# Kernel tuning notes

Hardware: AMD Instinct MI355X
Metric: run time of the kernel (lower is better)

## Reference

```python
import jax, jax.numpy as jnp
import numpy as np

MODEL_DIM = 2048
NUM_HEADS = 16
HEAD_DIM = MODEL_DIM // NUM_HEADS  # 128
B, L = 2, 2048


def _rope_tables(seq_len, head_dim, theta=10000.0):
    inv = 1.0 / (theta ** (np.arange(0, head_dim, 2)[: head_dim // 2].astype(np.float32) / head_dim))
    t = np.arange(seq_len, dtype=np.float32)
    freqs = np.outer(t, inv)  # [L, head_dim//2]
    return jnp.asarray(np.cos(freqs)), jnp.asarray(np.sin(freqs))


def setup_inputs() -> dict:
    key = jax.random.key(0)
    k1, k2, k3 = jax.random.split(key, 3)
    x = jax.random.normal(k1, (B, L, MODEL_DIM), dtype=jnp.float32)
    Wqkv = jax.random.normal(k2, (MODEL_DIM, 3 * MODEL_DIM), dtype=jnp.float32) / np.sqrt(MODEL_DIM)
    Wc = jax.random.normal(k3, (MODEL_DIM, MODEL_DIM), dtype=jnp.float32) / np.sqrt(MODEL_DIM)
    bc = jnp.zeros((MODEL_DIM,), dtype=jnp.float32)
    freqs_cos, freqs_sin = _rope_tables(L, HEAD_DIM)
    return {"x": x, "freqs_cos": freqs_cos, "freqs_sin": freqs_sin,
            "Wqkv": Wqkv, "Wc": Wc, "bc": bc}


def _apply_rope(t, cos, sin):
    # t: [B, L, H, hd] viewed as pairs (even, odd) along last dim; complex multiply by cis
    b, l, h, d = t.shape
    tp = t.reshape(b, l, h, d // 2, 2)
    te, to = tp[..., 0], tp[..., 1]
    cos = cos[None, :, None, :]  # [1, L, 1, d/2]
    sin = sin[None, :, None, :]
    oe = te * cos - to * sin
    oo = te * sin + to * cos
    return jnp.stack([oe, oo], axis=-1).reshape(b, l, h, d)


def reference(x, freqs_cos, freqs_sin, Wqkv, Wc, bc):
    b, l, d = x.shape
    qkv = x @ Wqkv  # [B, L, 3D]
    q, k, v = jnp.split(qkv, 3, axis=-1)
    q = q.reshape(b, l, NUM_HEADS, HEAD_DIM)
    k = k.reshape(b, l, NUM_HEADS, HEAD_DIM)
    v = v.reshape(b, l, NUM_HEADS, HEAD_DIM)
    q = _apply_rope(q, freqs_cos, freqs_sin)
    k = _apply_rope(k, freqs_cos, freqs_sin)
    scale = 1.0 / np.sqrt(HEAD_DIM).astype(np.float32)
    # causal SDPA: [B, H, Lq, Lk]
    scores = jnp.einsum('bqhd,bkhd->bhqk', q, k) * scale
    causal = jnp.tril(jnp.ones((l, l), dtype=bool))
    scores = jnp.where(causal[None, None], scores, jnp.finfo(scores.dtype).min)
    attn = jax.nn.softmax(scores, axis=-1)
    out = jnp.einsum('bhqk,bkhd->bqhd', attn, v).reshape(b, l, d)
    return out @ Wc + bc
```

## Files before the change

### kernel.cpp

```cpp
#include <hip/hip_runtime.h>
#include <hip/hip_bf16.h>

#define MODEL 2048
#define NHEAD 16
#define HDIM  128
#define BB    2
#define LL    2048
#define N1    (3*MODEL)
#define MTOT  (BB*LL)

typedef __hip_bfloat16 bf16;
typedef __attribute__((ext_vector_type(8))) short bf16x8;
typedef __attribute__((ext_vector_type(4))) float f32x4;

static __device__ __forceinline__ f32x4 mfma16(bf16x8 a, bf16x8 b, f32x4 c) {
  return __builtin_amdgcn_mfma_f32_16x16x32_bf16(a, b, c, 0, 0, 0);
}

static __device__ __forceinline__ void gl_lds16(const void* g, void* l) {
  __builtin_amdgcn_global_load_lds(
      (const __attribute__((address_space(1))) unsigned int*)g,
      (__attribute__((address_space(3))) unsigned int*)l, 16, 0, 0);
}

static __device__ __forceinline__ unsigned bfu(float x) {
  bf16 b = __float2bfloat16(x);
  return (unsigned)*reinterpret_cast<unsigned short*>(&b);
}

__global__ void k_cvt(const float* __restrict__ in, bf16* __restrict__ out, int n4) {
  int i = blockIdx.x * blockDim.x + threadIdx.x;
  if (i < n4) {
    float4 v = ((const float4*)in)[i];
    bf16* o = out + (size_t)i * 4;
    o[0] = __float2bfloat16(v.x);
    o[1] = __float2bfloat16(v.y);
    o[2] = __float2bfloat16(v.z);
    o[3] = __float2bfloat16(v.w);
  }
}

__global__ __launch_bounds__(256)
void k_transpose(const float* __restrict__ in, bf16* __restrict__ out, int R, int C) {
  __shared__ float t[32][33];
  const int c0 = blockIdx.x * 32, r0 = blockIdx.y * 32;
  const int tx = threadIdx.x & 31;
  const int ty = threadIdx.x >> 5;
#pragma unroll
  for (int i = 0; i < 4; ++i)
    t[ty + 8*i][tx] = in[(size_t)(r0 + ty + 8*i) * C + c0 + tx];
  __syncthreads();
#pragma unroll
  for (int i = 0; i < 4; ++i)
    out[(size_t)(c0 + ty + 8*i) * R + r0 + tx] = __float2bfloat16(t[tx][ty + 8*i]);
}


#define BARRIER __builtin_amdgcn_s_barrier()
#define SCHED0  __builtin_amdgcn_sched_barrier(0)
#define PRIO1 __builtin_amdgcn_s_setprio(1)
#define PRIO0 __builtin_amdgcn_s_setprio(0)

template<int EPI>
__global__ __launch_bounds__(512, 4)
void k_gemmP(const bf16* __restrict__ A, const bf16* __restrict__ BT,
             int M, int N, int K,
             float* __restrict__ Cout, const float* __restrict__ bias,
             bf16* __restrict__ Qb, bf16* __restrict__ Kb, bf16* __restrict__ VTb,
             const float* __restrict__ cosT, const float* __restrict__ sinT)
{
  constexpr int ABUF = 8192;
  constexpr int BBUF = 8192;
  constexpr int AREG = 3 * ABUF;
  extern __shared__ char smem[];

  const int tid = threadIdx.x;
  const int wid = tid >> 6, lane = tid & 63;
  const int wm = wid >> 2, wn = wid & 3;
  const int lr = lane & 15, lkg = lane >> 4;

  const int nbx = N >> 7;
  const int xcd = blockIdx.x & 7;
  const int i   = blockIdx.x >> 3;
  const int m0 = (((xcd >> 1) << 3) + (i & 7)) << 7;
  const int n0 = ((xcd & 1) * (nbx >> 1) + (i >> 3)) << 7;

  const int scol = ((lane & 3) ^ ((lane >> 3) & 3)) * 8;
  const bf16* Asrc = A  + (size_t)(m0 + wid*16 + (lane >> 2)) * K + scol;
  const bf16* Bsrc = BT + (size_t)(n0 + wid*16 + (lane >> 2)) * K + scol;

  auto stageA = [&](int t) {
    gl_lds16(Asrc + t*32, smem + (t % 3)*ABUF + wid*1024);
  };
  auto stageB = [&](int t) {
    gl_lds16(Bsrc + t*32, smem + AREG + (t % 3)*BBUF + wid*1024);
  };

  const int slotX = (lkg ^ ((lr >> 1) & 3)) * 16;
  const int aBase = wm*4096 + lr*64 + slotX;
  const int bBase = wn*2048 + lr*64 + slotX;

  const f32x4 vzero = {0.f, 0.f, 0.f, 0.f};
  f32x4 acc[4][2];
#pragma unroll
  for (int ii = 0; ii < 4; ++ii)
#pragma unroll
    for (int j = 0; j < 2; ++j) acc[ii][j] = vzero;

  const int nt = K >> 5;

  stageA(0); stageB(0); stageA(1); stageB(1);
  asm volatile("s_waitcnt vmcnt(2)" ::: "memory");
  SCHED0; BARRIER;

  for (int t = 0; t < nt; ++t) {
    const int bufA = (t % 3) * ABUF;
    const int bufB = AREG + (t % 3) * BBUF;
    const int ts   = (t + 2 < nt) ? t + 2 : nt - 1;
    bf16x8 aFr[4], bFr[2];

#pragma unroll
    for (int mf = 0; mf < 4; ++mf)
      aFr[mf] = *(const bf16x8*)(smem + bufA + aBase + mf*1024);
#pragma unroll
    for (int nf = 0; nf < 2; ++nf)
      bFr[nf] = *(const bf16x8*)(smem + bufB + bBase + nf*1024);
    stageA(ts); stageB(ts);

    asm volatile("s_waitcnt lgkmcnt(0)" ::: "memory");
    SCHED0;
    PRIO1;
#pragma unroll
    for (int mf = 0; mf < 4; ++mf)
#pragma unroll
      for (int nf = 0; nf < 2; ++nf)
        acc[mf][nf] = mfma16(aFr[mf], bFr[nf], acc[mf][nf]);
    PRIO0;
    asm volatile("s_waitcnt vmcnt(2)" ::: "memory");
    SCHED0;
    BARRIER;
  }

  if constexpr (EPI == 1) {
    const float inv_sqrt_d = 0.08838834764831845f;
#pragma unroll
    for (int nf = 0; nf < 2; ++nf) {
      const int gcb = n0 + wn*32 + nf*16;
      const int section = gcb >> 11;
      const int cc = (gcb & 2047) + lr;
      const int h = cc >> 7, d = cc & 127;
#pragma unroll
      for (int mf = 0; mf < 4; ++mf) {
#pragma unroll
        for (int reg = 0; reg < 4; ++reg) {
          const int grow = m0 + wm*64 + mf*16 + lkg*4 + reg;
          const int bidx = grow >> 11, lseq = grow & 2047;
          float val = acc[mf][nf][reg];
          if (section < 2) {
            float p = __shfl_xor(val, 1);
            const int fi = d >> 1;
            float cv = cosT[(size_t)lseq * 64 + fi];
            float sv = sinT[(size_t)lseq * 64 + fi];
            float r = (d & 1) ? fmaf(p, sv, val * cv)
                              : fmaf(val, cv, -p * sv);
            if (section == 0) {
              r *= inv_sqrt_d;
              Qb[((size_t)(bidx*NHEAD + h) * LL + lseq) * HDIM + d] = __float2bfloat16(r);
            } else {
              Kb[((size_t)(bidx*NHEAD + h) * LL + lseq) * HDIM + d] = __float2bfloat16(r);
            }
          } else {
            VTb[((size_t)(bidx*NHEAD + h) * HDIM + d) * LL + lseq] = __float2bfloat16(val);
          }
        }
      }
    }
  } else {
#pragma unroll
    for (int nf = 0; nf < 2; ++nf) {
      const int gcol = n0 + wn*32 + nf*16 + lr;
      const float bv = bias[gcol];
#pragma unroll
      for (int mf = 0; mf < 4; ++mf) {
#pragma unroll
        for (int reg = 0; reg < 4; ++reg) {
          const int grow = m0 + wm*64 + mf*16 + lkg*4 + reg;
          Cout[(size_t)grow * N + gcol] = acc[mf][nf][reg] + bv;
        }
      }
    }
  }
}

__global__ __launch_bounds__(256, 2)
void k_attn(const bf16* __restrict__ Qb, const bf16* __restrict__ Kb,
            const bf16* __restrict__ VTb, bf16* __restrict__ attnA)
{
  __shared__ bf16 Ks[64][136];
  __shared__ bf16 Vs[128][72];
  __shared__ bf16 Ps[4][32][72];

  const int bh  = blockIdx.y;
  const int bx  = blockIdx.x;
  const int tid = threadIdx.x;
  const int wid = tid >> 6, lane = tid & 63;
  const int lr  = lane & 15, lkg = lane >> 4;

  const bf16* Qh = Qb  + (size_t)bh * LL * HDIM;
  const bf16* Kh = Kb  + (size_t)bh * LL * HDIM;
  const bf16* Vh = VTb + (size_t)bh * HDIM * LL;
  const int b = bh >> 4, h = bh & 15;
  const f32x4 vzero = {0.f, 0.f, 0.f, 0.f};

  for (int pp = 0; pp < 2; ++pp) {
    const int qt  = pp ? bx : (15 - bx);
    const int Q0  = qt * 128;
    const int q0w = Q0 + wid * 32;

    bf16x8 qf[2][4];
#pragma unroll
    for (int qr = 0; qr < 2; ++qr)
#pragma unroll
      for (int kk = 0; kk < 4; ++kk)
        qf[qr][kk] = *(const bf16x8*)(Qh + (size_t)(q0w + qr*16 + lr) * HDIM + kk*32 + lkg*8);

    f32x4 oacc[2][8];
#pragma unroll
    for (int qr = 0; qr < 2; ++qr)
#pragma unroll
      for (int db = 0; db < 8; ++db) oacc[qr][db] = vzero;
    float ml[2] = {-INFINITY, -INFINITY};
    float ll[2] = {0.f, 0.f};

    const int NT = Q0 / 64 + 2;
    bf16x8 kpre[4], vpre[4];
#pragma unroll
    for (int j = 0; j < 4; ++j) {
      const int c = j*256 + tid;
      kpre[j] = *(const bf16x8*)(Kh + (size_t)(c >> 4) * HDIM + (c & 15) * 8);
      vpre[j] = *(const bf16x8*)(Vh + (size_t)(c >> 3) * LL + (c & 7) * 8);
    }

    for (int kt = 0; kt < NT; ++kt) {
      const int kbase = kt * 64;
      __syncthreads();
#pragma unroll
      for (int j = 0; j < 4; ++j) {
        const int c = j*256 + tid;
        *(bf16x8*)&Ks[c >> 4][(c & 15) * 8] = kpre[j];
        *(bf16x8*)&Vs[c >> 3][(c & 7) * 8]  = vpre[j];
      }
      __syncthreads();
      if (kt + 1 < NT) {
#pragma unroll
        for (int j = 0; j < 4; ++j) {
          const int c = j*256 + tid;
          kpre[j] = *(const bf16x8*)(Kh + (size_t)((kt+1)*64 + (c >> 4)) * HDIM + (c & 15) * 8);
          vpre[j] = *(const bf16x8*)(Vh + (size_t)(c >> 3) * LL + (kt+1)*64 + (c & 7) * 8);
        }
      }
      if (kbase <= q0w + 31) {
        f32x4 s2[2][4];
#pragma unroll
        for (int qr = 0; qr < 2; ++qr)
#pragma unroll
          for (int c = 0; c < 4; ++c) s2[qr][c] = vzero;
#pragma unroll
        for (int c = 0; c < 4; ++c) {
          bf16x8 kf[4];
#pragma unroll
          for (int kk = 0; kk < 4; ++kk)
            kf[kk] = *(const bf16x8*)&Ks[c*16 + lr][kk*32 + lkg*8];
#pragma unroll
          for (int qr = 0; qr < 2; ++qr)
#pragma unroll
            for (int kk = 0; kk < 4; ++kk)
              s2[qr][c] = mfma16(kf[kk], qf[qr][kk], s2[qr][c]);
        }
#pragma unroll
        for (int qr = 0; qr < 2; ++qr) {
          const int qrow = q0w + qr*16 + lr;
          float pv[4][4];
#pragma unroll
          for (int c = 0; c < 4; ++c)
#pragma unroll
            for (int reg = 0; reg < 4; ++reg) {
              const int kv = kbase + c*16 + lkg*4 + reg;
              pv[c][reg] = (kv <= qrow) ? s2[qr][c][reg] : -INFINITY;
            }
          float tm = pv[0][0];
#pragma unroll
          for (int c = 0; c < 4; ++c)
#pragma unroll
            for (int reg = 0; reg < 4; ++reg)
              if (c || reg) tm = fmaxf(tm, pv[c][reg]);
          tm = fmaxf(tm, __shfl_xor(tm, 16));
          tm = fmaxf(tm, __shfl_xor(tm, 32));
          const float mnew = fmaxf(ml[qr], tm);
          const float scl  = __expf(ml[qr] - mnew);
          ml[qr] = mnew;
          float rs = 0.f;
#pragma unroll
          for (int c = 0; c < 4; ++c)
#pragma unroll
            for (int reg = 0; reg < 4; ++reg) {
              pv[c][reg] = __expf(pv[c][reg] - mnew);
              rs += pv[c][reg];
            }
          rs += __shfl_xor(rs, 16);
          rs += __shfl_xor(rs, 32);
          ll[qr] = ll[qr] * scl + rs;
#pragma unroll
          for (int c = 0; c < 4; ++c) {
            unsigned lo = bfu(pv[c][0]) | (bfu(pv[c][1]) << 16);
            unsigned hi = bfu(pv[c][2]) | (bfu(pv[c][3]) << 16);
            *(uint2*)&Ps[wid][qr*16 + lr][c*16 + lkg*4] = make_uint2(lo, hi);
          }
          float sr[4];
#pragma unroll
          for (int reg = 0; reg < 4; ++reg) sr[reg] = __shfl(scl, lkg*4 + reg);
#pragma unroll
          for (int db = 0; db < 8; ++db) {
            oacc[qr][db][0] *= sr[0]; oacc[qr][db][1] *= sr[1];
            oacc[qr][db][2] *= sr[2]; oacc[qr][db][3] *= sr[3];
          }
        }
        asm volatile("s_waitcnt lgkmcnt(0)" ::: "memory");
        __builtin_amdgcn_sched_barrier(0);
        bf16x8 pf[2][2];
#pragma unroll
        for (int qr = 0; qr < 2; ++qr)
#pragma unroll
          for (int k2 = 0; k2 < 2; ++k2)
            pf[qr][k2] = *(const bf16x8*)&Ps[wid][qr*16 + lr][k2*32 + lkg*8];
#pragma unroll
        for (int db = 0; db < 8; ++db) {
          bf16x8 vf0 = *(const bf16x8*)&Vs[db*16 + lr][lkg*8];
          bf16x8 vf1 = *(const bf16x8*)&Vs[db*16 + lr][32 + lkg*8];
#pragma unroll
          for (int qr = 0; qr < 2; ++qr) {
            oacc[qr][db] = mfma16(pf[qr][0], vf0, oacc[qr][db]);
            oacc[qr][db] = mfma16(pf[qr][1], vf1, oacc[qr][db]);
          }
        }
      }
    }

#pragma unroll
    for (int qr = 0; qr < 2; ++qr) {
      const float myinv = 1.0f / ll[qr];
      float li[4];
#pragma unroll
      for (int reg = 0; reg < 4; ++reg) li[reg] = __shfl(myinv, lkg*4 + reg);
#pragma unroll
      for (int reg = 0; reg < 4; ++reg) {
        const int row = q0w + qr*16 + lkg*4 + reg;
        bf16* dst = attnA + ((size_t)(b*LL + row)) * MODEL + h * HDIM;
#pragma unroll
        for (int db = 0; db < 8; ++db)
          dst[db*16 + lr] = __float2bfloat16(oacc[qr][db][reg] * li[reg]);
      }
    }
  }
}

extern "C" void kernel_launch(void* const* d_in, const int* in_sizes, int n_in,
                              void* d_out, int out_size, void* d_ws, size_t ws_size,
                              hipStream_t stream)
{
  const float* x    = (const float*)d_in[0];
  const float* cosT = (const float*)d_in[1];
  const float* sinT = (const float*)d_in[2];
  const float* Wqkv = (const float*)d_in[3];
  const float* Wc   = (const float*)d_in[4];
  const float* bc   = (const float*)d_in[5];
  float* out = (float*)d_out;

  if (ws_size < 100663296u) return;
  char* w = (char*)d_ws;
  bf16* x16   = (bf16*)(w);
  bf16* WqkvT = (bf16*)(w + (size_t)16777216);
  bf16* WcT   = (bf16*)(w + (size_t)41943040);
  bf16* Qb    = (bf16*)(w + (size_t)50331648);
  bf16* Kb    = (bf16*)(w + (size_t)67108864);
  bf16* VTb   = (bf16*)(w + (size_t)83886080);
  bf16* attnA = x16;

  hipFuncSetAttribute(reinterpret_cast<const void*>(&k_gemmP<1>),
                      hipFuncAttributeMaxDynamicSharedMemorySize, 49152);
  hipFuncSetAttribute(reinterpret_cast<const void*>(&k_gemmP<2>),
                      hipFuncAttributeMaxDynamicSharedMemorySize, 49152);

  k_cvt<<<(MTOT*MODEL/4 + 255)/256, 256, 0, stream>>>(x, x16, MTOT*MODEL/4);
  k_transpose<<<dim3(N1/32,    MODEL/32), 256, 0, stream>>>(Wqkv, WqkvT, MODEL, N1);
  k_transpose<<<dim3(MODEL/32, MODEL/32), 256, 0, stream>>>(Wc,   WcT,   MODEL, MODEL);

  k_gemmP<1><<<(N1/128)*(MTOT/128), 512, 49152, stream>>>(
      x16, WqkvT, MTOT, N1, MODEL,
      nullptr, nullptr, Qb, Kb, VTb, cosT, sinT);

  k_attn<<<dim3(8, BB*NHEAD), 256, 0, stream>>>(Qb, Kb, VTb, attnA);

  k_gemmP<2><<<(MODEL/128)*(MTOT/128), 512, 49152, stream>>>(
      attnA, WcT, MTOT, MODEL, MODEL,
      out, bc, nullptr, nullptr, nullptr, nullptr, nullptr);
}
```

Measured before the change: 297.1 us.

## Use 256x256 tiles with K=64 double-buffered LDS for the QKV GEMM

Adds a new GEMM kernel for the QKV projection. Each block computes a 256x256 output tile with BK=64 stages, double-buffered in 128 KB of LDS, and each wave holds an 8x4 grid of MFMA accumulators. This raises arithmetic intensity and data reuse per LDS and global load, and halves the number of barriers per unit of K. The cost is lower occupancy (launch bounds 512,2 and large LDS), fewer blocks (384) on the device, and only double buffering with a full vmcnt(0) wait each iteration.

```diff
diff --git a/kernel.cpp b/kernel.cpp
--- a/kernel.cpp
+++ b/kernel.cpp
@@ -27,6 +27,11 @@
   bf16 b = __float2bfloat16(x);
   return (unsigned)*reinterpret_cast<unsigned short*>(&b);
 }
+
+#define BARRIER __builtin_amdgcn_s_barrier()
+#define SCHED0  __builtin_amdgcn_sched_barrier(0)
+#define PRIO1 __builtin_amdgcn_s_setprio(1)
+#define PRIO0 __builtin_amdgcn_s_setprio(0)
 
 __global__ void k_cvt(const float* __restrict__ in, bf16* __restrict__ out, int n4) {
   int i = blockIdx.x * blockDim.x + threadIdx.x;
@@ -55,88 +60,95 @@
     out[(size_t)(c0 + ty + 8*i) * R + r0 + tx] = __float2bfloat16(t[tx][ty + 8*i]);
 }
 
-
-#define BARRIER __builtin_amdgcn_s_barrier()
-#define SCHED0  __builtin_amdgcn_sched_barrier(0)
-#define PRIO1 __builtin_amdgcn_s_setprio(1)
-#define PRIO0 __builtin_amdgcn_s_setprio(0)
-
 template<int EPI>
-__global__ __launch_bounds__(512, 4)
-void k_gemmP(const bf16* __restrict__ A, const bf16* __restrict__ BT,
+__global__ __launch_bounds__(512, 2)
+void k_gemmX(const bf16* __restrict__ A, const bf16* __restrict__ BT,
              int M, int N, int K,
              float* __restrict__ Cout, const float* __restrict__ bias,
              bf16* __restrict__ Qb, bf16* __restrict__ Kb, bf16* __restrict__ VTb,
              const float* __restrict__ cosT, const float* __restrict__ sinT)
 {
-  constexpr int ABUF = 8192;
-  constexpr int BBUF = 8192;
-  constexpr int AREG = 3 * ABUF;
   extern __shared__ char smem[];
-
   const int tid = threadIdx.x;
   const int wid = tid >> 6, lane = tid & 63;
   const int wm = wid >> 2, wn = wid & 3;
   const int lr = lane & 15, lkg = lane >> 4;
 
-  const int nbx = N >> 7;
+  const int nby = M >> 8, nbx = N >> 8;
+  const int mc  = nby >> 2;
   const int xcd = blockIdx.x & 7;
   const int i   = blockIdx.x >> 3;
-  const int m0 = (((xcd >> 1) << 3) + (i & 7)) << 7;
-  const int n0 = ((xcd & 1) * (nbx >> 1) + (i >> 3)) << 7;
-
-  const int scol = ((lane & 3) ^ ((lane >> 3) & 3)) * 8;
-  const bf16* Asrc = A  + (size_t)(m0 + wid*16 + (lane >> 2)) * K + scol;
-  const bf16* Bsrc = BT + (size_t)(n0 + wid*16 + (lane >> 2)) * K + scol;
-
-  auto stageA = [&](int t) {
-    gl_lds16(Asrc + t*32, smem + (t % 3)*ABUF + wid*1024);
+  const int m0 = (((xcd >> 1) * mc) + (i % mc)) << 8;
+  const int n0 = (((xcd & 1) * (nbx >> 1)) + (i / mc)) << 8;
+
+  const int srow = lane >> 3;
+  const int scol = ((lane ^ (lane >> 3)) & 7) * 8;
+  const bf16* Asrc = A  + (size_t)(m0 + wid*8 + srow) * K + scol;
+  const bf16* Bsrc = BT + (size_t)(n0 + wid*8 + srow) * K + scol;
+
+  auto stage = [&](int t, int buf) {
+    const bf16* ga = Asrc + (size_t)t * 64;
+    const bf16* gb = Bsrc + (size_t)t * 64;
+    char* da = smem + buf*65536 + wid*1024;
+    char* db = smem + buf*65536 + 32768 + wid*1024;
+#pragma unroll
+    for (int j = 0; j < 4; ++j) {
+      gl_lds16(ga + (size_t)(64*j) * K, da + j*8192);
+      gl_lds16(gb + (size_t)(64*j) * K, db + j*8192);
+    }
   };
-  auto stageB = [&](int t) {
-    gl_lds16(Bsrc + t*32, smem + AREG + (t % 3)*BBUF + wid*1024);
-  };
-
-  const int slotX = (lkg ^ ((lr >> 1) & 3)) * 16;
-  const int aBase = wm*4096 + lr*64 + slotX;
-  const int bBase = wn*2048 + lr*64 + slotX;
+
+  const int swz = (lr & 7) << 4;
+  const int c0 = (lkg * 16) ^ swz;
+  const int c1 = (lkg * 16 + 64) ^ swz;
+  const int aRow = wm*16384 + lr*128;
+  const int bRow = 32768 + wn*8192 + lr*128;
 
   const f32x4 vzero = {0.f, 0.f, 0.f, 0.f};
-  f32x4 acc[4][2];
-#pragma unroll
-  for (int ii = 0; ii < 4; ++ii)
-#pragma unroll
-    for (int j = 0; j < 2; ++j) acc[ii][j] = vzero;
-
-  const int nt = K >> 5;
-
-  stageA(0); stageB(0); stageA(1); stageB(1);
-  asm volatile("s_waitcnt vmcnt(2)" ::: "memory");
+  f32x4 acc[8][4];
+#pragma unroll
+  for (int ii = 0; ii < 8; ++ii)
+#pragma unroll
+    for (int j = 0; j < 4; ++j) acc[ii][j] = vzero;
+
+  const int nt = K >> 6;
+
+  stage(0, 0);
+  asm volatile("s_waitcnt vmcnt(0)" ::: "memory");
   SCHED0; BARRIER;
 
   for (int t = 0; t < nt; ++t) {
-    const int bufA = (t % 3) * ABUF;
-    const int bufB = AREG + (t % 3) * BBUF;
-    const int ts   = (t + 2 < nt) ? t + 2 : nt - 1;
-    bf16x8 aFr[4], bFr[2];
-
-#pragma unroll
-    for (int mf = 0; mf < 4; ++mf)
-      aFr[mf] = *(const bf16x8*)(smem + bufA + aBase + mf*1024);
-#pragma unroll
-    for (int nf = 0; nf < 2; ++nf)
-      bFr[nf] = *(const bf16x8*)(smem + bufB + bBase + nf*1024);
-    stageA(ts); stageB(ts);
-
-    asm volatile("s_waitcnt lgkmcnt(0)" ::: "memory");
-    SCHED0;
+    const int buf = (t & 1) * 65536;
+    bf16x8 a0[8], b0[4], a1[8], b1[4];
+
+#pragma unroll
+    for (int mf = 0; mf < 8; ++mf)
+      a0[mf] = *(const bf16x8*)(smem + buf + aRow + mf*2048 + c0);
+#pragma unroll
+    for (int nf = 0; nf < 4; ++nf)
+      b0[nf] = *(const bf16x8*)(smem + buf + bRow + nf*2048 + c0);
+    if (t + 1 < nt) stage(t + 1, (t & 1) ^ 1);
     PRIO1;
 #pragma unroll
-    for (int mf = 0; mf < 4; ++mf)
-#pragma unroll
-      for (int nf = 0; nf < 2; ++nf)
-        acc[mf][nf] = mfma16(aFr[mf], bFr[nf], acc[mf][nf]);
+    for (int mf = 0; mf < 8; ++mf)
+#pragma unroll
+      for (int nf = 0; nf < 4; ++nf)
+        acc[mf][nf] = mfma16(a0[mf], b0[nf], acc[mf][nf]);
     PRIO0;
-    asm volatile("s_waitcnt vmcnt(2)" ::: "memory");
+#pragma unroll
+    for (int mf = 0; mf < 8; ++mf)
+      a1[mf] = *(const bf16x8*)(smem + buf + aRow + mf*2048 + c1);
+#pragma unroll
+    for (int nf = 0; nf < 4; ++nf)
+      b1[nf] = *(const bf16x8*)(smem + buf + bRow + nf*2048 + c1);
+    PRIO1;
+#pragma unroll
+    for (int mf = 0; mf < 8; ++mf)
+#pragma unroll
+      for (int nf = 0; nf < 4; ++nf)
+        acc[mf][nf] = mfma16(a1[mf], b1[nf], acc[mf][nf]);
+    PRIO0;
+    asm volatile("s_waitcnt vmcnt(0)" ::: "memory");
     SCHED0;
     BARRIER;
   }
@@ -144,16 +156,16 @@
   if constexpr (EPI == 1) {
     const float inv_sqrt_d = 0.08838834764831845f;
 #pragma unroll
-    for (int nf = 0; nf < 2; ++nf) {
-      const int gcb = n0 + wn*32 + nf*16;
+    for (int nf = 0; nf < 4; ++nf) {
+      const int gcb = n0 + wn*64 + nf*16;
       const int section = gcb >> 11;
       const int cc = (gcb & 2047) + lr;
       const int h = cc >> 7, d = cc & 127;
 #pragma unroll
-      for (int mf = 0; mf < 4; ++mf) {
+      for (int mf = 0; mf < 8; ++mf) {
 #pragma unroll
         for (int reg = 0; reg < 4; ++reg) {
-          const int grow = m0 + wm*64 + mf*16 + lkg*4 + reg;
+          const int grow = m0 + wm*128 + mf*16 + lkg*4 + reg;
           const int bidx = grow >> 11, lseq = grow & 2047;
           float val = acc[mf][nf][reg];
           if (section < 2) {
@@ -177,16 +189,110 @@
     }
   } else {
 #pragma unroll
-    for (int nf = 0; nf < 2; ++nf) {
-      const int gcol = n0 + wn*32 + nf*16 + lr;
+    for (int nf = 0; nf < 4; ++nf) {
+      const int gcol = n0 + wn*64 + nf*16 + lr;
       const float bv = bias[gcol];
 #pragma unroll
-      for (int mf = 0; mf < 4; ++mf) {
+      for (int mf = 0; mf < 8; ++mf) {
 #pragma unroll
         for (int reg = 0; reg < 4; ++reg) {
-          const int grow = m0 + wm*64 + mf*16 + lkg*4 + reg;
+          const int grow = m0 + wm*128 + mf*16 + lkg*4 + reg;
           Cout[(size_t)grow * N + gcol] = acc[mf][nf][reg] + bv;
         }
+      }
+    }
+  }
+}
+
+template<int EPI>
+__global__ __launch_bounds__(512, 4)
+void k_gemmP(const bf16* __restrict__ A, const bf16* __restrict__ BT,
+             int M, int N, int K,
+             float* __restrict__ Cout, const float* __restrict__ bias,
+             const float* __restrict__ unused1, const float* __restrict__ unused2)
+{
+  constexpr int ABUF = 8192;
+  constexpr int BBUF = 8192;
+  constexpr int AREG = 3 * ABUF;
+  extern __shared__ char smem[];
+
+  const int tid = threadIdx.x;
+  const int wid = tid >> 6, lane = tid & 63;
+  const int wm = wid >> 2, wn = wid & 3;
+  const int lr = lane & 15, lkg = lane >> 4;
+
+  const int nbx = N >> 7;
+  const int xcd = blockIdx.x & 7;
+  const int i   = blockIdx.x >> 3;
+  const int m0 = (((xcd >> 1) << 3) + (i & 7)) << 7;
+  const int n0 = ((xcd & 1) * (nbx >> 1) + (i >> 3)) << 7;
+
+  const int scol = ((lane & 3) ^ ((lane >> 3) & 3)) * 8;
+  const bf16* Asrc = A  + (size_t)(m0 + wid*16 + (lane >> 2)) * K + scol;
+  const bf16* Bsrc = BT + (size_t)(n0 + wid*16 + (lane >> 2)) * K + scol;
+
+  auto stageA = [&](int t) {
+    gl_lds16(Asrc + t*32, smem + (t % 3)*ABUF + wid*1024);
+  };
+  auto stageB = [&](int t) {
+    gl_lds16(Bsrc + t*32, smem + AREG + (t % 3)*BBUF + wid*1024);
+  };
+
+  const int slotX = (lkg ^ ((lr >> 1) & 3)) * 16;
+  const int aBase = wm*4096 + lr*64 + slotX;
+  const int bBase = wn*2048 + lr*64 + slotX;
+
+  const f32x4 vzero = {0.f, 0.f, 0.f, 0.f};
+  f32x4 acc[4][2];
+#pragma unroll
+  for (int ii = 0; ii < 4; ++ii)
+#pragma unroll
+    for (int j = 0; j < 2; ++j) acc[ii][j] = vzero;
+
+  const int nt = K >> 5;
+
+  stageA(0); stageB(0); stageA(1); stageB(1);
+  asm volatile("s_waitcnt vmcnt(2)" ::: "memory");
+  SCHED0; BARRIER;
+
+  for (int t = 0; t < nt; ++t) {
+    const int bufA = (t % 3) * ABUF;
+    const int bufB = AREG + (t % 3) * BBUF;
+    const int ts   = (t + 2 < nt) ? t + 2 : nt - 1;
+    bf16x8 aFr[4], bFr[2];
+
+#pragma unroll
+    for (int mf = 0; mf < 4; ++mf)
+      aFr[mf] = *(const bf16x8*)(smem + bufA + aBase + mf*1024);
+#pragma unroll
+    for (int nf = 0; nf < 2; ++nf)
+      bFr[nf] = *(const bf16x8*)(smem + bufB + bBase + nf*1024);
+    stageA(ts); stageB(ts);
+
+    asm volatile("s_waitcnt lgkmcnt(0)" ::: "memory");
+    SCHED0;
+    PRIO1;
+#pragma unroll
+    for (int mf = 0; mf < 4; ++mf)
+#pragma unroll
+      for (int nf = 0; nf < 2; ++nf)
+        acc[mf][nf] = mfma16(aFr[mf], bFr[nf], acc[mf][nf]);
+    PRIO0;
+    asm volatile("s_waitcnt vmcnt(2)" ::: "memory");
+    SCHED0;
+    BARRIER;
+  }
+
+#pragma unroll
+  for (int nf = 0; nf < 2; ++nf) {
+    const int gcol = n0 + wn*32 + nf*16 + lr;
+    const float bv = bias[gcol];
+#pragma unroll
+    for (int mf = 0; mf < 4; ++mf) {
+#pragma unroll
+      for (int reg = 0; reg < 4; ++reg) {
+        const int grow = m0 + wm*64 + mf*16 + lkg*4 + reg;
+        Cout[(size_t)grow * N + gcol] = acc[mf][nf][reg] + bv;
       }
     }
   }
@@ -386,8 +492,8 @@
   bf16* VTb   = (bf16*)(w + (size_t)83886080);
   bf16* attnA = x16;
 
-  hipFuncSetAttribute(reinterpret_cast<const void*>(&k_gemmP<1>),
-                      hipFuncAttributeMaxDynamicSharedMemorySize, 49152);
+  hipFuncSetAttribute(reinterpret_cast<const void*>(&k_gemmX<1>),
+                      hipFuncAttributeMaxDynamicSharedMemorySize, 131072);
   hipFuncSetAttribute(reinterpret_cast<const void*>(&k_gemmP<2>),
                       hipFuncAttributeMaxDynamicSharedMemorySize, 49152);
 
@@ -395,7 +501,7 @@
   k_transpose<<<dim3(N1/32,    MODEL/32), 256, 0, stream>>>(Wqkv, WqkvT, MODEL, N1);
   k_transpose<<<dim3(MODEL/32, MODEL/32), 256, 0, stream>>>(Wc,   WcT,   MODEL, MODEL);
 
-  k_gemmP<1><<<(N1/128)*(MTOT/128), 512, 49152, stream>>>(
+  k_gemmX<1><<<(MTOT/256)*(N1/256), 512, 131072, stream>>>(
       x16, WqkvT, MTOT, N1, MODEL,
       nullptr, nullptr, Qb, Kb, VTb, cosT, sinT);
 
@@ -403,5 +509,5 @@
 
   k_gemmP<2><<<(MODEL/128)*(MTOT/128), 512, 49152, stream>>>(
       attnA, WcT, MTOT, MODEL, MODEL,
-      out, bc, nullptr, nullptr, nullptr, nullptr, nullptr);
-}
+      out, bc, nullptr, nullptr);
+}
```

Measured after the change: 316.2 us. 6.4% more time.
